# Kernel tuning notes

Measured on AMD Instinct MI355X. Metric: run time of the kernel, lower is better.

The kernel has to match this reference:

```python
import jax, jax.numpy as jnp
import numpy as np

B, S, E, WIN = 8, 2048, 512, 11  # batch, seq_len, emb_dim, window_size (odd)
PAD_VAL = 0.0  # padding_idx used as constant pad value in F.pad


def setup_inputs() -> dict:
    key = jax.random.key(0)
    k1, k2, k3 = jax.random.split(key, 3)
    x = jax.random.normal(k1, (B, S, E), dtype=jnp.float32)
    lim = 1.0 / np.sqrt(E * WIN)  # torch Linear default init bound
    # One independent Linear per timestep (deepcopy clones): stacked weights/bias
    W = jax.random.uniform(k2, (S, WIN, WIN * E), minval=-lim, maxval=lim, dtype=jnp.float32)
    b = jax.random.uniform(k3, (S, WIN), minval=-lim, maxval=lim, dtype=jnp.float32)
    return {"x": x, "W": W, "b": b}


def reference(x, W, b):
    ww = WIN // 2
    # pad sequence dim on both sides with padding_idx
    padded = jnp.pad(x, ((0, 0), (ww, ww), (0, 0)), constant_values=PAD_VAL)  # [B, S+2ww, E]
    # gather all sliding windows at once: windows[b,t,j,:] = padded[b, t+j, :]
    idx = jnp.arange(S)[:, None] + jnp.arange(WIN)[None, :]
    windows = padded[:, idx, :]
    flat = windows.reshape(B, S, WIN * E)                     # flattened window per position
    gates = jax.nn.sigmoid(jnp.einsum('bsf,swf->bsw', flat, W) + b)
    # gate * embeddings, sum over window, tanh
    score = jnp.einsum('bsw,bswe->bse', gates, windows)       # [B, S, E]
    return jnp.tanh(score)
```

## Files before the change

### kernel.cpp

```cpp
#include <hip/hip_runtime.h>
#include <math.h>

#define B_    8
#define S_    2048
#define E_    512
#define WIN_  11
#define WW    5
#define F4C   1408
#define E4C   128
#define PSTR  (B_ * WIN_)

template <int CTRL, int RMASK>
__device__ __forceinline__ float dpp_add(float v) {
    int sh = __builtin_amdgcn_update_dpp(0, __float_as_int(v),
                                         CTRL, RMASK, 0xF, true);
    return v + __int_as_float(sh);
}
__device__ __forceinline__ float wave_sum63(float v) {
    v = dpp_add<0x111, 0xF>(v);
    v = dpp_add<0x112, 0xF>(v);
    v = dpp_add<0x114, 0xF>(v);
    v = dpp_add<0x118, 0xF>(v);
    v = dpp_add<0x142, 0xA>(v);
    v = dpp_add<0x143, 0xC>(v);
    return v;
}

__device__ __forceinline__ float tanh_fast(float v) {
    const float e = __expf(v + v);
    return 1.f - 2.f / (e + 1.f);
}

__global__ __launch_bounds__(256)
void win_attn_fused(const float* __restrict__ x,
                    const float* __restrict__ W,
                    const float* __restrict__ bias,
                    float* __restrict__ out)
{
    const int bid  = blockIdx.x;
    const int s    = (bid & 7) * (S_ / 8) + (bid >> 3);
    const int tid  = threadIdx.x;
    const int wid  = tid >> 6;
    const int lane = tid & 63;

    const float4* __restrict__ X4 = reinterpret_cast<const float4*>(x);
    const float4* __restrict__ Ws = reinterpret_cast<const float4*>(W)
                                    + (size_t)s * (WIN_ * F4C);

    __shared__ float4 Wbuf[WIN_ * E4C];
    __shared__ float gates[PSTR];

    const int w0   = wid * 3;
    const int wcnt = (wid == 3) ? 2 : 3;

    float acc[B_][3];
    #pragma unroll
    for (int b = 0; b < B_; ++b)
        #pragma unroll
        for (int j = 0; j < 3; ++j) acc[b][j] = 0.f;

    #pragma unroll 1
    for (int wp = 0; wp < WIN_; ++wp) {
        #pragma unroll
        for (int j = 0; j < 6; ++j) {
            const int m = j * 256 + tid;
            if (j < 5 || wid < 2) {
                const int w  = m >> 7;
                const int e4 = m & 127;
                const float4* src = Ws + (size_t)w * F4C + wp * E4C + e4;
                __builtin_amdgcn_global_load_lds(
                    (const __attribute__((address_space(1))) void*)src,
                    (__attribute__((address_space(3))) void*)&Wbuf[m],
                    16, 0, 0);
            }
        }
        __syncthreads();

        const int row = s - WW + wp;
        if (row >= 0 && row < S_) {
            float4 wv[3][2];
            #pragma unroll
            for (int j = 0; j < 3; ++j)
                if (j < wcnt) {
                    wv[j][0] = Wbuf[(w0 + j) * E4C + lane];
                    wv[j][1] = Wbuf[(w0 + j) * E4C + lane + 64];
                }

            #pragma unroll
            for (int half = 0; half < 2; ++half) {
                float4 xv[4][2];
                #pragma unroll
                for (int bb = 0; bb < 4; ++bb) {
                    const int b = half * 4 + bb;
                    xv[bb][0] = X4[((size_t)b * S_ + row) * E4C + lane];
                    xv[bb][1] = X4[((size_t)b * S_ + row) * E4C + lane + 64];
                }
                #pragma unroll
                for (int bb = 0; bb < 4; ++bb) {
                    const int b = half * 4 + bb;
                    #pragma unroll
                    for (int j = 0; j < 3; ++j) {
                        if (j < wcnt) {
                            float a = acc[b][j];
                            a = fmaf(xv[bb][0].x, wv[j][0].x, a);
                            a = fmaf(xv[bb][0].y, wv[j][0].y, a);
                            a = fmaf(xv[bb][0].z, wv[j][0].z, a);
                            a = fmaf(xv[bb][0].w, wv[j][0].w, a);
                            a = fmaf(xv[bb][1].x, wv[j][1].x, a);
                            a = fmaf(xv[bb][1].y, wv[j][1].y, a);
                            a = fmaf(xv[bb][1].z, wv[j][1].z, a);
                            a = fmaf(xv[bb][1].w, wv[j][1].w, a);
                            acc[b][j] = a;
                        }
                    }
                }
            }
        }
        __syncthreads();
    }

    #pragma unroll
    for (int b = 0; b < B_; ++b)
        #pragma unroll
        for (int j = 0; j < 3; ++j)
            if (j < wcnt) acc[b][j] = wave_sum63(acc[b][j]);

    if (lane == 63) {
        #pragma unroll
        for (int b = 0; b < B_; ++b)
            #pragma unroll
            for (int j = 0; j < 3; ++j)
                if (j < wcnt) gates[b * WIN_ + w0 + j] = acc[b][j];
    }
    __syncthreads();

    if (tid < PSTR) {
        const int w = tid % WIN_;
        const float v = gates[tid] + bias[s * WIN_ + w];
        gates[tid] = 1.f / (1.f + __expf(-v));
    }
    __syncthreads();

    float4* __restrict__ OUT4 = reinterpret_cast<float4*>(out);
    #pragma unroll
    for (int it = 0; it < 4; ++it) {
        const int i  = tid + (it << 8);
        const int b  = i >> 7;
        const int e4 = i & 127;
        float4 sc = make_float4(0.f, 0.f, 0.f, 0.f);
        #pragma unroll
        for (int w = 0; w < WIN_; ++w) {
            const int r = s - WW + w;
            if (r >= 0 && r < S_) {
                const float g   = gates[b * WIN_ + w];
                const float4 xv = X4[((size_t)b * S_ + r) * E4C + e4];
                sc.x = fmaf(g, xv.x, sc.x);
                sc.y = fmaf(g, xv.y, sc.y);
                sc.z = fmaf(g, xv.z, sc.z);
                sc.w = fmaf(g, xv.w, sc.w);
            }
        }
        float4 o;
        o.x = tanh_fast(sc.x);
        o.y = tanh_fast(sc.y);
        o.z = tanh_fast(sc.z);
        o.w = tanh_fast(sc.w);
        OUT4[((size_t)b * S_ + s) * E4C + e4] = o;
    }
}

extern "C" void kernel_launch(void* const* d_in, const int* in_sizes, int n_in,
                              void* d_out, int out_size, void* d_ws, size_t ws_size,
                              hipStream_t stream)
{
    const float* x    = (const float*)d_in[0];
    const float* W    = (const float*)d_in[1];
    const float* bias = (const float*)d_in[2];
    float* out        = (float*)d_out;

    win_attn_fused<<<dim3(S_), dim3(256), 0, stream>>>(x, W, bias, out);
}
```

Measured before the change: 156.0 us.

## Double-buffer per-window weight staging in LDS and batch all x row loads

The weight-slice staging buffer becomes two LDS buffers. The next window position's weights are fetched asynchronously into one buffer while the current position is computed from the other, which removes one barrier per iteration and is meant to hide weight-load latency. All 8 batch rows of x are now loaded at once instead of in two halves of four, adding more loads in flight at the cost of more registers. The doubled LDS footprint and the in-order vmcnt waits caused by the later x loads may limit the overlap and reduce occupancy.

New measurement: 155.8 us. No clear change (-0.1%).

```diff
diff --git a/kernel.cpp b/kernel.cpp
--- a/kernel.cpp
+++ b/kernel.cpp
@@ -47,20 +47,13 @@
     const float4* __restrict__ Ws = reinterpret_cast<const float4*>(W)
                                     + (size_t)s * (WIN_ * F4C);
 
-    __shared__ float4 Wbuf[WIN_ * E4C];
+    __shared__ float4 Wbuf[2][WIN_ * E4C];
     __shared__ float gates[PSTR];
 
     const int w0   = wid * 3;
     const int wcnt = (wid == 3) ? 2 : 3;
 
-    float acc[B_][3];
-    #pragma unroll
-    for (int b = 0; b < B_; ++b)
-        #pragma unroll
-        for (int j = 0; j < 3; ++j) acc[b][j] = 0.f;
-
-    #pragma unroll 1
-    for (int wp = 0; wp < WIN_; ++wp) {
+    auto STAGE = [&](int buf, int wp) {
         #pragma unroll
         for (int j = 0; j < 6; ++j) {
             const int m = j * 256 + tid;
@@ -70,53 +63,65 @@
                 const float4* src = Ws + (size_t)w * F4C + wp * E4C + e4;
                 __builtin_amdgcn_global_load_lds(
                     (const __attribute__((address_space(1))) void*)src,
-                    (__attribute__((address_space(3))) void*)&Wbuf[m],
+                    (__attribute__((address_space(3))) void*)&Wbuf[buf][m],
                     16, 0, 0);
             }
         }
-        __syncthreads();
+    };
+
+    float acc[B_][3];
+    #pragma unroll
+    for (int b = 0; b < B_; ++b)
+        #pragma unroll
+        for (int j = 0; j < 3; ++j) acc[b][j] = 0.f;
+
+    if (s - WW >= 0) STAGE(0, 0);
+    __syncthreads();
+
+    int cur = 0;
+    #pragma unroll 1
+    for (int wp = 0; wp < WIN_; ++wp) {
+        if (wp + 1 < WIN_) {
+            const int nrow = s - WW + (wp + 1);
+            if (nrow >= 0 && nrow < S_) STAGE(cur ^ 1, wp + 1);
+        }
 
         const int row = s - WW + wp;
         if (row >= 0 && row < S_) {
+            float4 xv[B_][2];
+            #pragma unroll
+            for (int b = 0; b < B_; ++b) {
+                xv[b][0] = X4[((size_t)b * S_ + row) * E4C + lane];
+                xv[b][1] = X4[((size_t)b * S_ + row) * E4C + lane + 64];
+            }
+
             float4 wv[3][2];
             #pragma unroll
             for (int j = 0; j < 3; ++j)
                 if (j < wcnt) {
-                    wv[j][0] = Wbuf[(w0 + j) * E4C + lane];
-                    wv[j][1] = Wbuf[(w0 + j) * E4C + lane + 64];
+                    wv[j][0] = Wbuf[cur][(w0 + j) * E4C + lane];
+                    wv[j][1] = Wbuf[cur][(w0 + j) * E4C + lane + 64];
                 }
 
             #pragma unroll
-            for (int half = 0; half < 2; ++half) {
-                float4 xv[4][2];
+            for (int b = 0; b < B_; ++b)
                 #pragma unroll
-                for (int bb = 0; bb < 4; ++bb) {
-                    const int b = half * 4 + bb;
-                    xv[bb][0] = X4[((size_t)b * S_ + row) * E4C + lane];
-                    xv[bb][1] = X4[((size_t)b * S_ + row) * E4C + lane + 64];
-                }
-                #pragma unroll
-                for (int bb = 0; bb < 4; ++bb) {
-                    const int b = half * 4 + bb;
-                    #pragma unroll
-                    for (int j = 0; j < 3; ++j) {
-                        if (j < wcnt) {
-                            float a = acc[b][j];
-                            a = fmaf(xv[bb][0].x, wv[j][0].x, a);
-                            a = fmaf(xv[bb][0].y, wv[j][0].y, a);
-                            a = fmaf(xv[bb][0].z, wv[j][0].z, a);
-                            a = fmaf(xv[bb][0].w, wv[j][0].w, a);
-                            a = fmaf(xv[bb][1].x, wv[j][1].x, a);
-                            a = fmaf(xv[bb][1].y, wv[j][1].y, a);
-                            a = fmaf(xv[bb][1].z, wv[j][1].z, a);
-                            a = fmaf(xv[bb][1].w, wv[j][1].w, a);
-                            acc[b][j] = a;
-                        }
+                for (int j = 0; j < 3; ++j)
+                    if (j < wcnt) {
+                        float a = acc[b][j];
+                        a = fmaf(xv[b][0].x, wv[j][0].x, a);
+                        a = fmaf(xv[b][0].y, wv[j][0].y, a);
+                        a = fmaf(xv[b][0].z, wv[j][0].z, a);
+                        a = fmaf(xv[b][0].w, wv[j][0].w, a);
+                        a = fmaf(xv[b][1].x, wv[j][1].x, a);
+                        a = fmaf(xv[b][1].y, wv[j][1].y, a);
+                        a = fmaf(xv[b][1].z, wv[j][1].z, a);
+                        a = fmaf(xv[b][1].w, wv[j][1].w, a);
+                        acc[b][j] = a;
                     }
-                }
-            }
         }
         __syncthreads();
+        cur ^= 1;
     }
 
     #pragma unroll
```
